# Kernel optimization log

Hardware: AMD Instinct MI355X
Metric: run time of the kernel (lower is better)

Reference implementation:

```python
import jax, jax.numpy as jnp
import numpy as np

B, N, D_MEM, D_HID = 64, 65536, 1024, 1024


def setup_inputs() -> dict:
    key = jax.random.key(0)
    k1, k2, k3 = jax.random.split(key, 3)
    memory_bank = jax.random.normal(k1, (N, D_MEM), dtype=jnp.float32)
    decoder_state = jax.random.normal(k2, (B, D_HID), dtype=jnp.float32)
    # nn.Linear(memory_bank_size -> hidden_size, bias=False): weight [D_HID, D_MEM]
    W = jax.random.normal(k3, (D_HID, D_MEM), dtype=jnp.float32) / np.sqrt(D_MEM)
    # ragged tree sizes summing exactly to N (concrete, built on host)
    rng = np.random.default_rng(0)
    lens = rng.integers(512, 1536, size=B).astype(np.float64)
    lens = np.maximum(1, np.floor(lens * N / lens.sum()).astype(np.int64))
    lens[-1] += N - lens.sum()
    return {
        "memory_bank": memory_bank,
        "decoder_state": decoder_state,
        "W": W,
        "tree_node_num_lst": jnp.asarray(lens, dtype=jnp.int64),
    }


def reference(memory_bank, decoder_state, W, tree_node_num_lst):
    # segment id per node: tree index it belongs to (total_repeat_length keeps it jit-able)
    n_total = memory_bank.shape[0]
    batch = decoder_state.shape[0]
    seg = jnp.repeat(jnp.arange(batch), tree_node_num_lst, total_repeat_length=n_total)  # [N]
    # memory_project: one big GEMM instead of per-tree launches
    enc = memory_bank @ W.T                                  # [N, D_HID]
    # per-node score = <decoder_state[tree], enc[node]>
    scores = jnp.sum(enc * decoder_state[seg], axis=-1)      # [N]
    # segment (per-tree) stable softmax
    m = jax.ops.segment_max(scores, seg, num_segments=batch)  # [B]
    e = jnp.exp(scores - m[seg])                              # [N]
    z = jax.ops.segment_sum(e, seg, num_segments=batch)       # [B]
    attn = e / z[seg]                                         # [N]
    # context = attn-weighted sum of raw memory bank per tree
    context = jax.ops.segment_sum(attn[:, None] * memory_bank, seg, num_segments=batch)  # [B, D_MEM]
    return context
```

## Files before the change

kernel.cpp:

```cpp
#include <hip/hip_runtime.h>
#include <math.h>

#define B_TREES 64
#define N_NODES 65536
#define D 1024
#define D4 (D/4)

#define CHUNK 64
#define SUB 8
#define NSUB (CHUNK/SUB)
#define NCHUNK (N_NODES/CHUNK)
#define NSLOT (2*NCHUNK)
#define VZ 8

__device__ __forceinline__ void block_offsets(const int* __restrict__ lens32,
                                              int* __restrict__ soff,
                                              int tid, int lane) {
    if ((tid >> 6) == 0) {
        long long x32 = (long long)lens32[lane];
        long long tot = x32;
        #pragma unroll
        for (int o = 32; o > 0; o >>= 1) tot += __shfl_xor(tot, o, 64);
        int len = (tot == (long long)N_NODES) ? (int)x32
                                              : (int)(((const long long*)lens32)[lane]);
        int scan = len;
        #pragma unroll
        for (int o = 1; o < 64; o <<= 1) {
            int y = __shfl_up(scan, o, 64);
            if (lane >= o) scan += y;
        }
        soff[lane + 1] = scan;
        if (lane == 0) soff[0] = 0;
    }
}

__global__ __launch_bounds__(256) void v_kernel(const float* __restrict__ ds,
                                                const float* __restrict__ W,
                                                float* __restrict__ v_part) {
    const int m  = blockIdx.x * 256 + threadIdx.x;
    const int b0 = blockIdx.y * 4;
    const int z  = blockIdx.z;
    const int h0 = z * 128;
    float acc[4] = {0.f, 0.f, 0.f, 0.f};
    for (int h = h0; h < h0 + 128; ++h) {
        float wv = W[h * D + m];
        #pragma unroll
        for (int j = 0; j < 4; ++j)
            acc[j] += ds[(b0 + j) * D + h] * wv;
    }
    #pragma unroll
    for (int j = 0; j < 4; ++j)
        v_part[((size_t)(z * B_TREES + b0 + j)) * D + m] = acc[j];
}

__global__ __launch_bounds__(256, 4) void fused_kernel(
    const float4* __restrict__ mb, const float4* __restrict__ v_part,
    const int* __restrict__ lens32,
    float* __restrict__ m_arr, float* __restrict__ z_arr,
    int* __restrict__ seg_arr, float4* __restrict__ vec)
{
    __shared__ float4 smb[SUB * D4];
    __shared__ float  ssc[SUB];
    __shared__ int    soff[B_TREES + 1];

    const int tid  = threadIdx.x;
    const int wave = tid >> 6;
    const int lane = tid & 63;
    const int c    = blockIdx.x;
    const int n0   = c * CHUNK;

    float4 pf[SUB];
    #pragma unroll
    for (int k = 0; k < SUB; ++k)
        pf[k] = mb[(size_t)(n0 + k) * D4 + tid];

    block_offsets(lens32, soff, tid, lane);
    __syncthreads();

    int lo = 0, hi = B_TREES - 1;
    while (lo < hi) { int mid = (lo + hi + 1) >> 1; if (soff[mid] <= n0) lo = mid; else hi = mid - 1; }
    const int sa   = lo;
    const int nxt  = soff[sa + 1];
    const int cutg = (nxt < n0 + CHUNK) ? nxt : 0x7fffffff;
    const bool two = (cutg != 0x7fffffff);

    float  m0 = -INFINITY, z0 = 0.f, m1 = -INFINITY, z1 = 0.f;
    float4 a0 = make_float4(0.f, 0.f, 0.f, 0.f);
    float4 a1 = make_float4(0.f, 0.f, 0.f, 0.f);

    float4 vr0, vr1, vr2, vr3;
    int vcur = -1;

    for (int st = 0; st < NSUB; ++st) {
        const int nb = n0 + st * SUB;

        #pragma unroll
        for (int k = 0; k < SUB; ++k)
            smb[k * D4 + tid] = pf[k];
        __syncthreads();

        if (st + 1 < NSUB) {
            const int nb2 = nb + SUB;
            #pragma unroll
            for (int k = 0; k < SUB; ++k)
                pf[k] = mb[(size_t)(nb2 + k) * D4 + tid];
        }

        #pragma unroll
        for (int q = 0; q < 2; ++q) {
            const int k  = wave * 2 + q;
            const int sg = (nb + k < cutg) ? sa : sa + 1;
            if (sg != vcur) {
                vcur = sg;
                vr0 = make_float4(0.f,0.f,0.f,0.f); vr1 = vr0; vr2 = vr0; vr3 = vr0;
                #pragma unroll
                for (int z = 0; z < VZ; ++z) {
                    const float4* vp = v_part + (size_t)(z * B_TREES + sg) * D4;
                    float4 t;
                    t = vp[  0 + lane]; vr0.x+=t.x; vr0.y+=t.y; vr0.z+=t.z; vr0.w+=t.w;
                    t = vp[ 64 + lane]; vr1.x+=t.x; vr1.y+=t.y; vr1.z+=t.z; vr1.w+=t.w;
                    t = vp[128 + lane]; vr2.x+=t.x; vr2.y+=t.y; vr2.z+=t.z; vr2.w+=t.w;
                    t = vp[192 + lane]; vr3.x+=t.x; vr3.y+=t.y; vr3.z+=t.z; vr3.w+=t.w;
                }
            }
            const float4 b0v = smb[k * D4 +   0 + lane];
            const float4 b1v = smb[k * D4 +  64 + lane];
            const float4 b2v = smb[k * D4 + 128 + lane];
            const float4 b3v = smb[k * D4 + 192 + lane];
            float acc = b0v.x*vr0.x + b0v.y*vr0.y + b0v.z*vr0.z + b0v.w*vr0.w;
            acc      += b1v.x*vr1.x + b1v.y*vr1.y + b1v.z*vr1.z + b1v.w*vr1.w;
            acc      += b2v.x*vr2.x + b2v.y*vr2.y + b2v.z*vr2.z + b2v.w*vr2.w;
            acc      += b3v.x*vr3.x + b3v.y*vr3.y + b3v.z*vr3.z + b3v.w*vr3.w;
            #pragma unroll
            for (int o = 32; o > 0; o >>= 1) acc += __shfl_down(acc, o, 64);
            if (lane == 0) ssc[k] = acc;
        }
        __syncthreads();

        #pragma unroll
        for (int k = 0; k < SUB; ++k) {
            const float  s    = ssc[k];
            const float4 arow = smb[k * D4 + tid];
            if (nb + k < cutg) {
                if (s > m0) {
                    const float sc = __expf(m0 - s);
                    z0 *= sc; a0.x *= sc; a0.y *= sc; a0.z *= sc; a0.w *= sc;
                    m0 = s;
                }
                const float w = __expf(s - m0);
                z0 += w;
                a0.x += w * arow.x; a0.y += w * arow.y; a0.z += w * arow.z; a0.w += w * arow.w;
            } else {
                if (s > m1) {
                    const float sc = __expf(m1 - s);
                    z1 *= sc; a1.x *= sc; a1.y *= sc; a1.z *= sc; a1.w *= sc;
                    m1 = s;
                }
                const float w = __expf(s - m1);
                z1 += w;
                a1.x += w * arow.x; a1.y += w * arow.y; a1.z += w * arow.z; a1.w += w * arow.w;
            }
        }
        __syncthreads();
    }

    const int slot0 = 2 * c, slot1 = 2 * c + 1;
    vec[(size_t)slot0 * D4 + tid] = a0;
    if (tid == 0) { m_arr[slot0] = m0; z_arr[slot0] = z0; seg_arr[slot0] = sa; }
    if (two) {
        vec[(size_t)slot1 * D4 + tid] = a1;
        if (tid == 0) { m_arr[slot1] = m1; z_arr[slot1] = z1; seg_arr[slot1] = sa + 1; }
    } else if (tid == 0) {
        seg_arr[slot1] = -1;
    }
}

__global__ __launch_bounds__(256) void combine_kernel(
    const int* __restrict__ lens32, const float* __restrict__ m_arr,
    const float* __restrict__ z_arr, const int* __restrict__ seg_arr,
    const float4* __restrict__ vec, float4* __restrict__ out)
{
    __shared__ int soff[B_TREES + 1];
    const int t = threadIdx.x, lane = t & 63;
    block_offsets(lens32, soff, t, lane);
    __syncthreads();

    const int b  = blockIdx.x;
    const int s0 = soff[b], s1 = soff[b + 1];
    const int c0 = s0 / CHUNK, c1 = (s1 - 1) / CHUNK;

    float mseg = -INFINITY;
    for (int cc = c0; cc <= c1; ++cc) {
        #pragma unroll
        for (int j = 0; j < 2; ++j) {
            const int sl = 2 * cc + j;
            if (seg_arr[sl] == b) mseg = fmaxf(mseg, m_arr[sl]);
        }
    }
    float zseg = 0.f;
    float4 acc = make_float4(0.f, 0.f, 0.f, 0.f);
    for (int cc = c0; cc <= c1; ++cc) {
        #pragma unroll
        for (int j = 0; j < 2; ++j) {
            const int sl = 2 * cc + j;
            if (seg_arr[sl] == b) {
                const float sc = __expf(m_arr[sl] - mseg);
                zseg += sc * z_arr[sl];
                const float4 vv = vec[(size_t)sl * D4 + t];
                acc.x += sc * vv.x; acc.y += sc * vv.y;
                acc.z += sc * vv.z; acc.w += sc * vv.w;
            }
        }
    }
    const float inv = 1.f / zseg;
    acc.x *= inv; acc.y *= inv; acc.z *= inv; acc.w *= inv;
    out[(size_t)b * D4 + t] = acc;
}

extern "C" void kernel_launch(void* const* d_in, const int* in_sizes, int n_in,
                              void* d_out, int out_size, void* d_ws, size_t ws_size,
                              hipStream_t stream) {
    const float* mb   = (const float*)d_in[0];
    const float* ds   = (const float*)d_in[1];
    const float* W    = (const float*)d_in[2];
    const int*   lens = (const int*)d_in[3];
    float*       out  = (float*)d_out;

    char*  ws      = (char*)d_ws;
    float* v_part  = (float*)ws;
    float* m_arr   = (float*)(ws + (size_t)VZ * B_TREES * D * 4);
    float* z_arr   = m_arr + NSLOT;
    int*   seg_arr = (int*)(z_arr + NSLOT);
    float* vec     = (float*)((char*)(seg_arr + NSLOT));

    {
        dim3 grid(4, 16, VZ);
        v_kernel<<<grid, 256, 0, stream>>>(ds, W, v_part);
    }

    fused_kernel<<<NCHUNK, 256, 0, stream>>>(
        (const float4*)mb, (const float4*)v_part, lens,
        m_arr, z_arr, seg_arr, (float4*)vec);

    combine_kernel<<<B_TREES, 256, 0, stream>>>(
        lens, m_arr, z_arr, seg_arr, (const float4*)vec, (float4*)out);
}
```

Baseline: 431.2 us.

## Keep memory rows in registers and reduce scores across waves via small LDS buffer

Each thread now holds its float4 slice of every row in the sub-chunk in registers, instead of staging rows through shared memory where each wave computed whole-row dot products. Partial dots are computed per thread against the projected decoder vector, reduced within each wave with xor shuffles, then combined across the four waves through a double-buffered shared array, so only one barrier is needed per sub-step. The projected vectors for both possible trees are summed once up front rather than reloaded on each segment change. The explicit register prefetch of the next sub-chunk is dropped, so the kernel now depends on occupancy to hide global load latency, and it does more shuffle reductions (eight per wave per sub-step).

```diff
diff --git a/kernel.cpp b/kernel.cpp
--- a/kernel.cpp
+++ b/kernel.cpp
@@ -59,20 +59,14 @@
     float* __restrict__ m_arr, float* __restrict__ z_arr,
     int* __restrict__ seg_arr, float4* __restrict__ vec)
 {
-    __shared__ float4 smb[SUB * D4];
-    __shared__ float  ssc[SUB];
-    __shared__ int    soff[B_TREES + 1];
+    __shared__ float red[2][4][SUB];
+    __shared__ int   soff[B_TREES + 1];
 
     const int tid  = threadIdx.x;
     const int wave = tid >> 6;
     const int lane = tid & 63;
     const int c    = blockIdx.x;
     const int n0   = c * CHUNK;
-
-    float4 pf[SUB];
-    #pragma unroll
-    for (int k = 0; k < SUB; ++k)
-        pf[k] = mb[(size_t)(n0 + k) * D4 + tid];
 
     block_offsets(lens32, soff, tid, lane);
     __syncthreads();
@@ -84,84 +78,94 @@
     const int cutg = (nxt < n0 + CHUNK) ? nxt : 0x7fffffff;
     const bool two = (cutg != 0x7fffffff);
 
+    float4 vA = make_float4(0.f, 0.f, 0.f, 0.f);
+    #pragma unroll
+    for (int z = 0; z < VZ; ++z) {
+        const float4 t4 = v_part[(size_t)(z * B_TREES + sa) * D4 + tid];
+        vA.x += t4.x; vA.y += t4.y; vA.z += t4.z; vA.w += t4.w;
+    }
+    float4 vB = vA;
+    if (two) {
+        vB = make_float4(0.f, 0.f, 0.f, 0.f);
+        #pragma unroll
+        for (int z = 0; z < VZ; ++z) {
+            const float4 t4 = v_part[(size_t)(z * B_TREES + sa + 1) * D4 + tid];
+            vB.x += t4.x; vB.y += t4.y; vB.z += t4.z; vB.w += t4.w;
+        }
+    }
+
     float  m0 = -INFINITY, z0 = 0.f, m1 = -INFINITY, z1 = 0.f;
     float4 a0 = make_float4(0.f, 0.f, 0.f, 0.f);
     float4 a1 = make_float4(0.f, 0.f, 0.f, 0.f);
 
-    float4 vr0, vr1, vr2, vr3;
-    int vcur = -1;
-
     for (int st = 0; st < NSUB; ++st) {
         const int nb = n0 + st * SUB;
 
+        float4 m4[SUB];
         #pragma unroll
         for (int k = 0; k < SUB; ++k)
-            smb[k * D4 + tid] = pf[k];
+            m4[k] = mb[(size_t)(nb + k) * D4 + tid];
+
+        float p[SUB];
+        if (nb + SUB <= cutg) {
+            #pragma unroll
+            for (int k = 0; k < SUB; ++k)
+                p[k] = m4[k].x*vA.x + m4[k].y*vA.y + m4[k].z*vA.z + m4[k].w*vA.w;
+        } else if (nb >= cutg) {
+            #pragma unroll
+            for (int k = 0; k < SUB; ++k)
+                p[k] = m4[k].x*vB.x + m4[k].y*vB.y + m4[k].z*vB.z + m4[k].w*vB.w;
+        } else {
+            #pragma unroll
+            for (int k = 0; k < SUB; ++k) {
+                const float4 vk = (nb + k < cutg) ? vA : vB;
+                p[k] = m4[k].x*vk.x + m4[k].y*vk.y + m4[k].z*vk.z + m4[k].w*vk.w;
+            }
+        }
+
+        #pragma unroll
+        for (int k = 0; k < SUB; ++k) {
+            #pragma unroll
+            for (int o = 32; o > 0; o >>= 1)
+                p[k] += __shfl_xor(p[k], o, 64);
+        }
+
+        const int par = st & 1;
+        if (lane == 0) {
+            #pragma unroll
+            for (int k = 0; k < SUB; ++k) red[par][wave][k] = p[k];
+        }
         __syncthreads();
-
-        if (st + 1 < NSUB) {
-            const int nb2 = nb + SUB;
-            #pragma unroll
-            for (int k = 0; k < SUB; ++k)
-                pf[k] = mb[(size_t)(nb2 + k) * D4 + tid];
-        }
-
-        #pragma unroll
-        for (int q = 0; q < 2; ++q) {
-            const int k  = wave * 2 + q;
-            const int sg = (nb + k < cutg) ? sa : sa + 1;
-            if (sg != vcur) {
-                vcur = sg;
-                vr0 = make_float4(0.f,0.f,0.f,0.f); vr1 = vr0; vr2 = vr0; vr3 = vr0;
-                #pragma unroll
-                for (int z = 0; z < VZ; ++z) {
-                    const float4* vp = v_part + (size_t)(z * B_TREES + sg) * D4;
-                    float4 t;
-                    t = vp[  0 + lane]; vr0.x+=t.x; vr0.y+=t.y; vr0.z+=t.z; vr0.w+=t.w;
-                    t = vp[ 64 + lane]; vr1.x+=t.x; vr1.y+=t.y; vr1.z+=t.z; vr1.w+=t.w;
-                    t = vp[128 + lane]; vr2.x+=t.x; vr2.y+=t.y; vr2.z+=t.z; vr2.w+=t.w;
-                    t = vp[192 + lane]; vr3.x+=t.x; vr3.y+=t.y; vr3.z+=t.z; vr3.w+=t.w;
+        float s[SUB];
+        #pragma unroll
+        for (int k = 0; k < SUB; ++k)
+            s[k] = red[par][0][k] + red[par][1][k] + red[par][2][k] + red[par][3][k];
+
+        #pragma unroll
+        for (int k = 0; k < SUB; ++k) {
+            const float sc_ = s[k];
+            if (nb + k < cutg) {
+                if (sc_ > m0) {
+                    const float r = __expf(m0 - sc_);
+                    z0 *= r; a0.x *= r; a0.y *= r; a0.z *= r; a0.w *= r;
+                    m0 = sc_;
                 }
+                const float w = __expf(sc_ - m0);
+                z0 += w;
+                a0.x += w * m4[k].x; a0.y += w * m4[k].y;
+                a0.z += w * m4[k].z; a0.w += w * m4[k].w;
+            } else {
+                if (sc_ > m1) {
+                    const float r = __expf(m1 - sc_);
+                    z1 *= r; a1.x *= r; a1.y *= r; a1.z *= r; a1.w *= r;
+                    m1 = sc_;
+                }
+                const float w = __expf(sc_ - m1);
+                z1 += w;
+                a1.x += w * m4[k].x; a1.y += w * m4[k].y;
+                a1.z += w * m4[k].z; a1.w += w * m4[k].w;
             }
-            const float4 b0v = smb[k * D4 +   0 + lane];
-            const float4 b1v = smb[k * D4 +  64 + lane];
-            const float4 b2v = smb[k * D4 + 128 + lane];
-            const float4 b3v = smb[k * D4 + 192 + lane];
-            float acc = b0v.x*vr0.x + b0v.y*vr0.y + b0v.z*vr0.z + b0v.w*vr0.w;
-            acc      += b1v.x*vr1.x + b1v.y*vr1.y + b1v.z*vr1.z + b1v.w*vr1.w;
-            acc      += b2v.x*vr2.x + b2v.y*vr2.y + b2v.z*vr2.z + b2v.w*vr2.w;
-            acc      += b3v.x*vr3.x + b3v.y*vr3.y + b3v.z*vr3.z + b3v.w*vr3.w;
-            #pragma unroll
-            for (int o = 32; o > 0; o >>= 1) acc += __shfl_down(acc, o, 64);
-            if (lane == 0) ssc[k] = acc;
-        }
-        __syncthreads();
-
-        #pragma unroll
-        for (int k = 0; k < SUB; ++k) {
-            const float  s    = ssc[k];
-            const float4 arow = smb[k * D4 + tid];
-            if (nb + k < cutg) {
-                if (s > m0) {
-                    const float sc = __expf(m0 - s);
-                    z0 *= sc; a0.x *= sc; a0.y *= sc; a0.z *= sc; a0.w *= sc;
-                    m0 = s;
-                }
-                const float w = __expf(s - m0);
-                z0 += w;
-                a0.x += w * arow.x; a0.y += w * arow.y; a0.z += w * arow.z; a0.w += w * arow.w;
-            } else {
-                if (s > m1) {
-                    const float sc = __expf(m1 - s);
-                    z1 *= sc; a1.x *= sc; a1.y *= sc; a1.z *= sc; a1.w *= sc;
-                    m1 = s;
-                }
-                const float w = __expf(s - m1);
-                z1 += w;
-                a1.x += w * arow.x; a1.y += w * arow.y; a1.z += w * arow.z; a1.w += w * arow.w;
-            }
-        }
-        __syncthreads();
+        }
     }
 
     const int slot0 = 2 * c, slot1 = 2 * c + 1;
```

Result: faster. 399.5 us (-7.4%).
